# Kernel optimization log

Measured on AMD Instinct MI355X. Metric: run time of the kernel, lower is better.

## Reference

```python
import jax, jax.numpy as jnp
import numpy as np

N = 100000   # nodes
C = 128      # channels
K = 16       # clusters
E = 3200000  # edges (avg degree 32)


def setup_inputs() -> dict:
    key = jax.random.key(0)
    k1, k2, k3, k4 = jax.random.split(key, 4)
    features = jax.random.normal(k1, (N, C), dtype=jnp.float32)
    edge_row = jax.random.randint(k2, (E,), 0, N, dtype=jnp.int32)
    edge_col = jax.random.randint(k3, (E,), 0, N, dtype=jnp.int32)
    edge_val = jnp.ones((E,), dtype=jnp.float32)
    # orthogonal-ish init for fc weight (matches nn.init.orthogonal_ in spirit)
    w = jax.random.normal(k4, (K, C), dtype=jnp.float32)
    q, _ = jnp.linalg.qr(w.T)          # [C, K], orthonormal columns
    fc_w = q.T.astype(jnp.float32)     # [K, C]
    fc_b = jnp.zeros((K,), dtype=jnp.float32)
    return {"features": features, "edge_row": edge_row, "edge_col": edge_col,
            "edge_val": edge_val, "fc_w": fc_w, "fc_b": fc_b}


def reference(features, edge_row, edge_col, edge_val, fc_w, fc_b):
    collapse_regularization = 1.0
    n_nodes = features.shape[0]
    n_clusters = fc_w.shape[0]

    # assignments = softmax(Linear(features))  -> [N, K]
    assignments = jax.nn.softmax(features @ fc_w.T + fc_b, axis=1)
    cluster_sizes = jnp.sum(assignments, axis=0)            # [K]
    assignments_pooling = assignments / cluster_sizes       # [N, K]

    # degrees = column sums of sparse adjacency (no densification)
    degrees = jax.ops.segment_sum(edge_val, edge_col, num_segments=n_nodes)  # [N]
    number_of_edges = jnp.sum(degrees)

    # sparse A @ assignments via segment_sum over edges -> [N, K]
    a_s = jax.ops.segment_sum(edge_val[:, None] * assignments[edge_col],
                              edge_row, num_segments=n_nodes)
    graph_pooled = a_s.T @ assignments                      # S^T A S, [K, K]

    normalizer_left = assignments.T @ degrees[:, None]      # [K, 1]
    normalizer_right = degrees[None, :] @ assignments       # [1, K]
    normalizer = (normalizer_left @ normalizer_right) / 2.0 / number_of_edges

    spectral_loss = -jnp.trace(graph_pooled - normalizer) / 2.0 / number_of_edges
    sk = np.sqrt(n_clusters).astype(np.float32)
    collapse_loss = (jnp.sum(jnp.abs(cluster_sizes - n_nodes / n_clusters))
                     / n_nodes * sk / (sk - 1.0) / 2.0)
    loss = spectral_loss + collapse_regularization * collapse_loss

    features_pooled = jax.nn.selu(assignments_pooling.T @ features)  # [K, C]
    features_pooled = assignments_pooling @ features_pooled          # unpool [N, C]
    return features_pooled, assignments, loss
```

## Files before the change

### kernel.cpp

```cpp
#include <hip/hip_runtime.h>
#include <hip/hip_fp16.h>
#include <math.h>


#define WS_ESUM 0
#define WS_TR   1
#define WS_M    2
#define WS_CS   18
#define WS_B    64

#define OFF_AH  0
#define OFF_CSP 800000
#define OFF_EP  825008
#define OFF_BP  861872

#define GE_BLOCKS 2048
#define GB_BLOCKS 512

typedef int   int4v   __attribute__((ext_vector_type(4)));
typedef float float2v __attribute__((ext_vector_type(2)));
typedef float float4v __attribute__((ext_vector_type(4)));

__global__ __launch_bounds__(256) void k_assign(
    const float* __restrict__ F, const float* __restrict__ W,
    const float* __restrict__ bias, float* __restrict__ A,
    __half* __restrict__ Ah, float* __restrict__ csp, int N) {
  __shared__ float Ws[16 * 144];
  __shared__ float csred[4][16];
  int t = threadIdx.x;
#pragma unroll
  for (int i = 0; i < 8; i++) {
    int idx = t + 256 * i;
    int k = idx >> 7, r = idx & 127;
    Ws[k * 144 + (r >> 5) * 36 + (r & 31)] = W[idx];
  }
  __syncthreads();

  int p = t & 3;
  int slot = t >> 2;
  int n0 = blockIdx.x * 128 + slot;
  int n1 = n0 + 64;
  bool act0 = (n0 < N), act1 = (n1 < N);
  int n0c = act0 ? n0 : (N - 1);
  int n1c = act1 ? n1 : (N - 1);

  float a0[16], a1[16];
#pragma unroll
  for (int k = 0; k < 16; k++) { a0[k] = 0.f; a1[k] = 0.f; }

  const float4* f0 = (const float4*)(F + (size_t)n0c * 128 + p * 32);
  const float4* f1 = (const float4*)(F + (size_t)n1c * 128 + p * 32);
#pragma unroll
  for (int i = 0; i < 8; i++) {
    float4 x0 = f0[i];
    float4 x1 = f1[i];
#pragma unroll
    for (int k = 0; k < 16; k++) {
      float4 w = *(const float4*)(&Ws[k * 144 + p * 36 + i * 4]);
      a0[k] = fmaf(x0.x, w.x, a0[k]);
      a0[k] = fmaf(x0.y, w.y, a0[k]);
      a0[k] = fmaf(x0.z, w.z, a0[k]);
      a0[k] = fmaf(x0.w, w.w, a0[k]);
      a1[k] = fmaf(x1.x, w.x, a1[k]);
      a1[k] = fmaf(x1.y, w.y, a1[k]);
      a1[k] = fmaf(x1.z, w.z, a1[k]);
      a1[k] = fmaf(x1.w, w.w, a1[k]);
    }
  }

#pragma unroll
  for (int k = 0; k < 16; k++) {
    a0[k] += __shfl_xor(a0[k], 1, 64);
    a0[k] += __shfl_xor(a0[k], 2, 64);
    a1[k] += __shfl_xor(a1[k], 1, 64);
    a1[k] += __shfl_xor(a1[k], 2, 64);
  }

#pragma unroll
  for (int k = 0; k < 16; k++) { a0[k] += bias[k]; a1[k] += bias[k]; }

  float mx0 = a0[0], mx1 = a1[0];
#pragma unroll
  for (int k = 1; k < 16; k++) { mx0 = fmaxf(mx0, a0[k]); mx1 = fmaxf(mx1, a1[k]); }
  float s0 = 0.f, s1 = 0.f;
#pragma unroll
  for (int k = 0; k < 16; k++) {
    a0[k] = __expf(a0[k] - mx0); s0 += a0[k];
    a1[k] = __expf(a1[k] - mx1); s1 += a1[k];
  }
  float inv0 = 1.0f / s0, inv1 = 1.0f / s1;
#pragma unroll
  for (int k = 0; k < 16; k++) { a0[k] *= inv0; a1[k] *= inv1; }

  if (act0)
    ((float4*)(A + (size_t)n0 * 16))[p] =
        make_float4(a0[p * 4 + 0], a0[p * 4 + 1], a0[p * 4 + 2], a0[p * 4 + 3]);
  if (act1)
    ((float4*)(A + (size_t)n1 * 16))[p] =
        make_float4(a1[p * 4 + 0], a1[p * 4 + 1], a1[p * 4 + 2], a1[p * 4 + 3]);

  if (p == 0 && act0) {
    __half2 hh[4];
    hh[0].x = __float2half_rn(a0[0]); hh[0].y = __float2half_rn(a0[1]);
    hh[1].x = __float2half_rn(a0[2]); hh[1].y = __float2half_rn(a0[3]);
    hh[2].x = __float2half_rn(a0[4]); hh[2].y = __float2half_rn(a0[5]);
    hh[3].x = __float2half_rn(a0[6]); hh[3].y = __float2half_rn(a0[7]);
    *(uint4*)(Ah + (size_t)n0 * 16) = *(uint4*)hh;
  } else if (p == 1 && act0) {
    __half2 hh[4];
    hh[0].x = __float2half_rn(a0[8]);  hh[0].y = __float2half_rn(a0[9]);
    hh[1].x = __float2half_rn(a0[10]); hh[1].y = __float2half_rn(a0[11]);
    hh[2].x = __float2half_rn(a0[12]); hh[2].y = __float2half_rn(a0[13]);
    hh[3].x = __float2half_rn(a0[14]); hh[3].y = __float2half_rn(a0[15]);
    *(uint4*)(Ah + (size_t)n0 * 16 + 8) = *(uint4*)hh;
  } else if (p == 2 && act1) {
    __half2 hh[4];
    hh[0].x = __float2half_rn(a1[0]); hh[0].y = __float2half_rn(a1[1]);
    hh[1].x = __float2half_rn(a1[2]); hh[1].y = __float2half_rn(a1[3]);
    hh[2].x = __float2half_rn(a1[4]); hh[2].y = __float2half_rn(a1[5]);
    hh[3].x = __float2half_rn(a1[6]); hh[3].y = __float2half_rn(a1[7]);
    *(uint4*)(Ah + (size_t)n1 * 16) = *(uint4*)hh;
  } else if (p == 3 && act1) {
    __half2 hh[4];
    hh[0].x = __float2half_rn(a1[8]);  hh[0].y = __float2half_rn(a1[9]);
    hh[1].x = __float2half_rn(a1[10]); hh[1].y = __float2half_rn(a1[11]);
    hh[2].x = __float2half_rn(a1[12]); hh[2].y = __float2half_rn(a1[13]);
    hh[3].x = __float2half_rn(a1[14]); hh[3].y = __float2half_rn(a1[15]);
    *(uint4*)(Ah + (size_t)n1 * 16 + 8) = *(uint4*)hh;
  }

  int lane = t & 63, wid = t >> 6;
#pragma unroll
  for (int k = 0; k < 16; k++) {
    float v = 0.f;
    if (p == 0) {
      if (act0) v += a0[k];
      if (act1) v += a1[k];
    }
    for (int off = 32; off; off >>= 1) v += __shfl_xor(v, off, 64);
    if (lane == 0) csred[wid][k] = v;
  }
  __syncthreads();
  if (t < 16)
    csp[(size_t)blockIdx.x * 16 + t] =
        csred[0][t] + csred[1][t] + csred[2][t] + csred[3][t];
}

union H2F4 { float4 f4; __half2 h2[4]; };

__device__ __forceinline__ void edge_body(
    const __half* __restrict__ Ah, int r, int c, float v,
    float& eS, float& tr, float* m) {
  const float4* pc = (const float4*)(Ah + (size_t)c * 16);
  const float4* pr = (const float4*)(Ah + (size_t)r * 16);
  H2F4 uc0, uc1, ur0, ur1;
  uc0.f4 = pc[0]; uc1.f4 = pc[1];
  ur0.f4 = pr[0]; ur1.f4 = pr[1];
  float cf[16], rf[16];
#pragma unroll
  for (int j = 0; j < 4; j++) {
    float2 f;
    f = __half22float2(uc0.h2[j]); cf[2 * j] = f.x; cf[2 * j + 1] = f.y;
    f = __half22float2(uc1.h2[j]); cf[8 + 2 * j] = f.x; cf[9 + 2 * j] = f.y;
    f = __half22float2(ur0.h2[j]); rf[2 * j] = f.x; rf[2 * j + 1] = f.y;
    f = __half22float2(ur1.h2[j]); rf[8 + 2 * j] = f.x; rf[9 + 2 * j] = f.y;
  }
  eS += v;
  float d = 0.f;
#pragma unroll
  for (int k = 0; k < 16; k++) {
    m[k] = fmaf(v, cf[k], m[k]);
    d = fmaf(rf[k], cf[k], d);
  }
  tr = fmaf(v, d, tr);
}

__global__ __launch_bounds__(256, 8) void k_edge_nodeB(
    const int* __restrict__ row, const int* __restrict__ col,
    const float* __restrict__ val, const __half* __restrict__ Ah,
    const float* __restrict__ F, const float* __restrict__ A,
    float* __restrict__ ep, float* __restrict__ bp, int E, int N) {
  __shared__ float red[4][18];
  int b = blockIdx.x;
  int t = threadIdx.x;
  bool isNode = ((b % 5) == 4);

  if (!isNode) {
    int eb = b - b / 5;
    float eS = 0.f, tr = 0.f;
    float m[16];
#pragma unroll
    for (int i = 0; i < 16; i++) m[i] = 0.f;

    int tid = eb * 256 + t;
    const int T = GE_BLOCKS * 256;
    int e = tid;
    for (; e + T < E; e += 2 * T) {
      int   r0 = __builtin_nontemporal_load(row + e);
      int   c0 = __builtin_nontemporal_load(col + e);
      int   r1 = __builtin_nontemporal_load(row + e + T);
      int   c1 = __builtin_nontemporal_load(col + e + T);
      float v0 = __builtin_nontemporal_load(val + e);
      float v1 = __builtin_nontemporal_load(val + e + T);
      edge_body(Ah, r0, c0, v0, eS, tr, m);
      edge_body(Ah, r1, c1, v1, eS, tr, m);
    }
    for (; e < E; e += T)
      edge_body(Ah, row[e], col[e], val[e], eS, tr, m);

    float vals[18];
    vals[0] = eS; vals[1] = tr;
#pragma unroll
    for (int i = 0; i < 16; i++) vals[2 + i] = m[i];
#pragma unroll
    for (int i = 0; i < 18; i++) {
      float v = vals[i];
      for (int off = 32; off; off >>= 1) v += __shfl_xor(v, off, 64);
      vals[i] = v;
    }
    int lane = t & 63, wid = t >> 6;
    if (lane == 0) {
#pragma unroll
      for (int i = 0; i < 18; i++) red[wid][i] = vals[i];
    }
    __syncthreads();
    if (t < 18)
      ep[(size_t)eb * 18 + t] =
          red[0][t] + red[1][t] + red[2][t] + red[3][t];
  } else {
    int nb = b / 5;
    int lane = t & 63;
    int wid = t >> 6;

    float2 acc[16];
#pragma unroll
    for (int k = 0; k < 16; k++) acc[k] = make_float2(0.f, 0.f);

    const float2v* F2 = (const float2v*)F;
    const float4* A4 = (const float4*)A;
    const int stride = GB_BLOCKS * 4;
    for (int n = nb * 4 + wid; n < N; n += stride) {
      float2v f = __builtin_nontemporal_load(&F2[(size_t)n * 64 + lane]);
      float4 a0 = A4[(size_t)n * 4 + 0];
      float4 a1 = A4[(size_t)n * 4 + 1];
      float4 a2 = A4[(size_t)n * 4 + 2];
      float4 a3 = A4[(size_t)n * 4 + 3];
      float av[16] = {a0.x, a0.y, a0.z, a0.w, a1.x, a1.y, a1.z, a1.w,
                      a2.x, a2.y, a2.z, a2.w, a3.x, a3.y, a3.z, a3.w};
#pragma unroll
      for (int k = 0; k < 16; k++) {
        acc[k].x = fmaf(av[k], f.x, acc[k].x);
        acc[k].y = fmaf(av[k], f.y, acc[k].y);
      }
    }
    float* myrow = bp + (size_t)(nb * 4 + wid) * 2048;
#pragma unroll
    for (int k = 0; k < 16; k++)
      *(float2*)&myrow[k * 128 + lane * 2] = acc[k];
  }
}

__global__ __launch_bounds__(256) void k_reduce(
    const float* __restrict__ csp, const float* __restrict__ ep,
    const float* __restrict__ bp, float* __restrict__ ws,
    int GA, int GE, int GB) {
  __shared__ float L[256];
  int t = threadIdx.x;
  int b = blockIdx.x;
  if (b < 256) {
    int cell = b * 8 + (t & 7);
    int seg = t >> 3;
    float s0 = 0.f, s1 = 0.f, s2 = 0.f, s3 = 0.f;
    int g = seg;
    for (; g + 96 < GB; g += 128) {
      s0 += bp[(size_t)g * 2048 + cell];
      s1 += bp[(size_t)(g + 32) * 2048 + cell];
      s2 += bp[(size_t)(g + 64) * 2048 + cell];
      s3 += bp[(size_t)(g + 96) * 2048 + cell];
    }
    for (; g < GB; g += 32) s0 += bp[(size_t)g * 2048 + cell];
    L[t] = (s0 + s1) + (s2 + s3);
    __syncthreads();
    if (t < 8) {
      float tot = 0.f;
#pragma unroll
      for (int s = 0; s < 32; s++) tot += L[s * 8 + t];
      ws[WS_B + b * 8 + t] = tot;
    }
  } else if (b == 256) {
    int n = GE * 18;
    float s0 = 0.f, s1 = 0.f, s2 = 0.f, s3 = 0.f;
    if (t < 252) {
      int f = t;
      for (; f + 756 < n; f += 1008) {
        s0 += ep[f]; s1 += ep[f + 252]; s2 += ep[f + 504]; s3 += ep[f + 756];
      }
      for (; f < n; f += 252) s0 += ep[f];
    }
    L[t] = (s0 + s1) + (s2 + s3);
    __syncthreads();
    if (t < 18) {
      float tot = 0.f;
#pragma unroll
      for (int j = 0; j < 14; j++) tot += L[j * 18 + t];
      ws[t] = tot;
    }
  } else {
    int n = GA * 16;
    float s0 = 0.f, s1 = 0.f, s2 = 0.f, s3 = 0.f;
    int f = t;
    for (; f + 768 < n; f += 1024) {
      s0 += csp[f]; s1 += csp[f + 256]; s2 += csp[f + 512]; s3 += csp[f + 768];
    }
    for (; f < n; f += 256) s0 += csp[f];
    L[t] = (s0 + s1) + (s2 + s3);
    __syncthreads();
    if (t < 16) {
      float tot = 0.f;
#pragma unroll
      for (int j = 0; j < 16; j++) tot += L[j * 16 + t];
      ws[WS_CS + t] = tot;
    }
  }
}

__global__ __launch_bounds__(256) void k_unpool(
    const float* __restrict__ A, float* __restrict__ ws,
    float* __restrict__ out, float* __restrict__ loss_out, int N) {
  __shared__ float Ps[2048];
  __shared__ float invcs[16];
  int t = threadIdx.x;
  if (t < 16) invcs[t] = 1.0f / ws[WS_CS + t];
  __syncthreads();
  const float scale = 1.0507009873554805f;
  const float alpha = 1.6732632423543772f;
#pragma unroll
  for (int i = 0; i < 8; i++) {
    int idx = t + 256 * i;
    int k = idx >> 7;
    float x = ws[WS_B + idx] * invcs[k];
    float s = (x > 0.f) ? scale * x : scale * alpha * expm1f(x);
    Ps[idx] = s * invcs[k];
  }
  __syncthreads();

  if (blockIdx.x == 0 && t == 0) {
    float Es = ws[WS_ESUM], tr = ws[WS_TR];
    float m2 = 0.f;
#pragma unroll
    for (int i = 0; i < 16; i++) m2 += ws[WS_M + i] * ws[WS_M + i];
    float spectral = -(tr - m2 / (2.0f * Es)) / (2.0f * Es);
    float coll = 0.f;
    float tgt = (float)N / 16.0f;
#pragma unroll
    for (int i = 0; i < 16; i++) coll += fabsf(ws[WS_CS + i] - tgt);
    coll = coll / (float)N * (4.0f / 3.0f / 2.0f);
    loss_out[0] = spectral + coll;
  }

  int c4 = (t & 31) << 2;
  int sub = t >> 5;
  float4 pk[16];
#pragma unroll
  for (int k = 0; k < 16; k++) pk[k] = *(const float4*)&Ps[k * 128 + c4];

  int stride = gridDim.x * 8;
  for (int n = blockIdx.x * 8 + sub; n < N; n += stride) {
    const float4* a4 = (const float4*)(A + (size_t)n * 16);
    float4 a0 = a4[0], a1 = a4[1], a2 = a4[2], a3 = a4[3];
    float av[16] = {a0.x, a0.y, a0.z, a0.w, a1.x, a1.y, a1.z, a1.w,
                    a2.x, a2.y, a2.z, a2.w, a3.x, a3.y, a3.z, a3.w};
    float4v s = {0.f, 0.f, 0.f, 0.f};
#pragma unroll
    for (int k = 0; k < 16; k++) {
      s.x = fmaf(av[k], pk[k].x, s.x);
      s.y = fmaf(av[k], pk[k].y, s.y);
      s.z = fmaf(av[k], pk[k].z, s.z);
      s.w = fmaf(av[k], pk[k].w, s.w);
    }
    __builtin_nontemporal_store(s, (float4v*)(out + (size_t)n * 128 + c4));
  }
}

extern "C" void kernel_launch(void* const* d_in, const int* in_sizes, int n_in,
                              void* d_out, int out_size, void* d_ws, size_t ws_size,
                              hipStream_t stream) {
  const float* F    = (const float*)d_in[0];
  const int*   erow = (const int*)d_in[1];
  const int*   ecol = (const int*)d_in[2];
  const float* eval_= (const float*)d_in[3];
  const float* W    = (const float*)d_in[4];
  const float* bias = (const float*)d_in[5];

  int N = in_sizes[0] / 128;
  int E = in_sizes[1];

  float* out0 = (float*)d_out;
  float* A    = out0 + (size_t)N * 128;
  float* loss = A + (size_t)N * 16;
  float* ws   = (float*)d_ws;

  int GA = (N + 127) / 128;
  int GE = GE_BLOCKS;
  int GBp = GB_BLOCKS * 4;

  __half* Ah  = (__half*)(out0 + OFF_AH);
  float*  csp = out0 + OFF_CSP;
  float*  ep  = out0 + OFF_EP;
  float*  bp  = out0 + OFF_BP;

  k_assign<<<GA, 256, 0, stream>>>(F, W, bias, A, Ah, csp, N);
  k_edge_nodeB<<<GE_BLOCKS + GB_BLOCKS, 256, 0, stream>>>(
      erow, ecol, eval_, Ah, F, A, ep, bp, E, N);
  k_reduce<<<258, 256, 0, stream>>>(csp, ep, bp, ws, GA, GE, GBp);
  k_unpool<<<1280, 256, 0, stream>>>(A, ws, out0, loss, N);
}
```

Before: 246.8 us.

## Split each edge across two lanes, each handling half of the cluster columns

Each edge is now processed by a pair of adjacent threads, each loading one 16-byte half of the row and column fp16 assignment vectors and accumulating 8 of the 16 cluster sums. This halves per-thread registers and gives more threads and memory requests in flight for the latency-bound gathers. In exchange, the row, col and val index loads are duplicated across the two lanes, and the reduction is restructured to keep the parities separate. eS is halved to correct for the double count.

```diff
diff --git a/kernel.cpp b/kernel.cpp
--- a/kernel.cpp
+++ b/kernel.cpp
@@ -148,27 +148,29 @@
 
 union H2F4 { float4 f4; __half2 h2[4]; };
 
-__device__ __forceinline__ void edge_body(
-    const __half* __restrict__ Ah, int r, int c, float v,
-    float& eS, float& tr, float* m) {
-  const float4* pc = (const float4*)(Ah + (size_t)c * 16);
-  const float4* pr = (const float4*)(Ah + (size_t)r * 16);
-  H2F4 uc0, uc1, ur0, ur1;
-  uc0.f4 = pc[0]; uc1.f4 = pc[1];
-  ur0.f4 = pr[0]; ur1.f4 = pr[1];
-  float cf[16], rf[16];
+__device__ __forceinline__ void pair_body(
+    const __half* __restrict__ Ah, const int* __restrict__ row,
+    const int* __restrict__ col, const float* __restrict__ val,
+    int e, int par, float& eS, float& tr, float* m) {
+  int   r = __builtin_nontemporal_load(row + e);
+  int   c = __builtin_nontemporal_load(col + e);
+  float v = __builtin_nontemporal_load(val + e);
+  const float4* pc = (const float4*)(Ah + ((size_t)c << 4) + (par << 3));
+  const float4* pr = (const float4*)(Ah + ((size_t)r << 4) + (par << 3));
+  H2F4 uc, ur;
+  uc.f4 = *pc;
+  ur.f4 = *pr;
+  float cf[8], rf[8];
 #pragma unroll
   for (int j = 0; j < 4; j++) {
     float2 f;
-    f = __half22float2(uc0.h2[j]); cf[2 * j] = f.x; cf[2 * j + 1] = f.y;
-    f = __half22float2(uc1.h2[j]); cf[8 + 2 * j] = f.x; cf[9 + 2 * j] = f.y;
-    f = __half22float2(ur0.h2[j]); rf[2 * j] = f.x; rf[2 * j + 1] = f.y;
-    f = __half22float2(ur1.h2[j]); rf[8 + 2 * j] = f.x; rf[9 + 2 * j] = f.y;
+    f = __half22float2(uc.h2[j]); cf[2 * j] = f.x; cf[2 * j + 1] = f.y;
+    f = __half22float2(ur.h2[j]); rf[2 * j] = f.x; rf[2 * j + 1] = f.y;
   }
   eS += v;
   float d = 0.f;
 #pragma unroll
-  for (int k = 0; k < 16; k++) {
+  for (int k = 0; k < 8; k++) {
     m[k] = fmaf(v, cf[k], m[k]);
     d = fmaf(rf[k], cf[k], d);
   }
@@ -187,41 +189,45 @@
 
   if (!isNode) {
     int eb = b - b / 5;
+    int par = t & 1;
     float eS = 0.f, tr = 0.f;
-    float m[16];
-#pragma unroll
-    for (int i = 0; i < 16; i++) m[i] = 0.f;
-
-    int tid = eb * 256 + t;
-    const int T = GE_BLOCKS * 256;
-    int e = tid;
-    for (; e + T < E; e += 2 * T) {
-      int   r0 = __builtin_nontemporal_load(row + e);
-      int   c0 = __builtin_nontemporal_load(col + e);
-      int   r1 = __builtin_nontemporal_load(row + e + T);
-      int   c1 = __builtin_nontemporal_load(col + e + T);
-      float v0 = __builtin_nontemporal_load(val + e);
-      float v1 = __builtin_nontemporal_load(val + e + T);
-      edge_body(Ah, r0, c0, v0, eS, tr, m);
-      edge_body(Ah, r1, c1, v1, eS, tr, m);
-    }
-    for (; e < E; e += T)
-      edge_body(Ah, row[e], col[e], val[e], eS, tr, m);
-
-    float vals[18];
-    vals[0] = eS; vals[1] = tr;
-#pragma unroll
-    for (int i = 0; i < 16; i++) vals[2 + i] = m[i];
-#pragma unroll
-    for (int i = 0; i < 18; i++) {
-      float v = vals[i];
-      for (int off = 32; off; off >>= 1) v += __shfl_xor(v, off, 64);
-      vals[i] = v;
+    float m[8];
+#pragma unroll
+    for (int i = 0; i < 8; i++) m[i] = 0.f;
+
+    int pid = eb * 128 + (t >> 1);
+    const int P = GE_BLOCKS * 128;
+    int e = pid;
+    for (; e + P < E; e += 2 * P) {
+      pair_body(Ah, row, col, val, e, par, eS, tr, m);
+      pair_body(Ah, row, col, val, e + P, par, eS, tr, m);
+    }
+    for (; e < E; e += P)
+      pair_body(Ah, row, col, val, e, par, eS, tr, m);
+
+#pragma unroll
+    for (int i = 0; i < 8; i++) {
+      float v = m[i];
+      v += __shfl_xor(v, 32, 64);
+      v += __shfl_xor(v, 16, 64);
+      v += __shfl_xor(v, 8, 64);
+      v += __shfl_xor(v, 4, 64);
+      v += __shfl_xor(v, 2, 64);
+      m[i] = v;
+    }
+    for (int off = 32; off; off >>= 1) {
+      eS += __shfl_xor(eS, off, 64);
+      tr += __shfl_xor(tr, off, 64);
     }
     int lane = t & 63, wid = t >> 6;
     if (lane == 0) {
-#pragma unroll
-      for (int i = 0; i < 18; i++) red[wid][i] = vals[i];
+      red[wid][0] = eS * 0.5f;
+      red[wid][1] = tr;
+#pragma unroll
+      for (int i = 0; i < 8; i++) red[wid][2 + i] = m[i];
+    } else if (lane == 1) {
+#pragma unroll
+      for (int i = 0; i < 8; i++) red[wid][10 + i] = m[i];
     }
     __syncthreads();
     if (t < 18)
```

Measured after the change: 248.2 us. About the same (+0.5%).

## Store assignment copy in FP8 for edge gathers and rebalance assign kernel

Applied to the files above, without the earlier changes.

The compact assignment copy used by the edge kernel is now packed as FP8 (16 bytes per node) instead of FP16 (32 bytes), which halves the random-gather traffic per edge endpoint and uses hardware pack/unpack conversions. k_assign now uses 8 threads per node pair with 64 nodes per block, so there are more blocks and each thread loads less data. The unpool grid is also enlarged. FP8 cuts precision of the trace term in the loss, which may hurt accuracy, and the grid changes alter csp sizing and the reduce partial count.

```diff
diff --git a/kernel.cpp b/kernel.cpp
--- a/kernel.cpp
+++ b/kernel.cpp
@@ -9,7 +9,7 @@
 #define WS_CS   18
 #define WS_B    64
 
-#define OFF_AH  0
+#define OFF_A8  0
 #define OFF_CSP 800000
 #define OFF_EP  825008
 #define OFF_BP  861872
@@ -17,29 +17,29 @@
 #define GE_BLOCKS 2048
 #define GB_BLOCKS 512
 
-typedef int   int4v   __attribute__((ext_vector_type(4)));
 typedef float float2v __attribute__((ext_vector_type(2)));
 typedef float float4v __attribute__((ext_vector_type(4)));
+typedef float f32x2   __attribute__((ext_vector_type(2)));
 
 __global__ __launch_bounds__(256) void k_assign(
     const float* __restrict__ F, const float* __restrict__ W,
     const float* __restrict__ bias, float* __restrict__ A,
-    __half* __restrict__ Ah, float* __restrict__ csp, int N) {
-  __shared__ float Ws[16 * 144];
+    unsigned char* __restrict__ A8, float* __restrict__ csp, int N) {
+  __shared__ float Ws[16 * 160];
   __shared__ float csred[4][16];
   int t = threadIdx.x;
 #pragma unroll
   for (int i = 0; i < 8; i++) {
     int idx = t + 256 * i;
     int k = idx >> 7, r = idx & 127;
-    Ws[k * 144 + (r >> 5) * 36 + (r & 31)] = W[idx];
+    Ws[k * 160 + (r >> 4) * 20 + (r & 15)] = W[idx];
   }
   __syncthreads();
 
-  int p = t & 3;
-  int slot = t >> 2;
-  int n0 = blockIdx.x * 128 + slot;
-  int n1 = n0 + 64;
+  int p = t & 7;
+  int slot = t >> 3;
+  int n0 = blockIdx.x * 64 + slot;
+  int n1 = n0 + 32;
   bool act0 = (n0 < N), act1 = (n1 < N);
   int n0c = act0 ? n0 : (N - 1);
   int n1c = act1 ? n1 : (N - 1);
@@ -48,15 +48,15 @@
 #pragma unroll
   for (int k = 0; k < 16; k++) { a0[k] = 0.f; a1[k] = 0.f; }
 
-  const float4* f0 = (const float4*)(F + (size_t)n0c * 128 + p * 32);
-  const float4* f1 = (const float4*)(F + (size_t)n1c * 128 + p * 32);
-#pragma unroll
-  for (int i = 0; i < 8; i++) {
+  const float4* f0 = (const float4*)(F + (size_t)n0c * 128 + p * 16);
+  const float4* f1 = (const float4*)(F + (size_t)n1c * 128 + p * 16);
+#pragma unroll
+  for (int i = 0; i < 4; i++) {
     float4 x0 = f0[i];
     float4 x1 = f1[i];
 #pragma unroll
     for (int k = 0; k < 16; k++) {
-      float4 w = *(const float4*)(&Ws[k * 144 + p * 36 + i * 4]);
+      float4 w = *(const float4*)(&Ws[k * 160 + p * 20 + i * 4]);
       a0[k] = fmaf(x0.x, w.x, a0[k]);
       a0[k] = fmaf(x0.y, w.y, a0[k]);
       a0[k] = fmaf(x0.z, w.z, a0[k]);
@@ -72,8 +72,10 @@
   for (int k = 0; k < 16; k++) {
     a0[k] += __shfl_xor(a0[k], 1, 64);
     a0[k] += __shfl_xor(a0[k], 2, 64);
+    a0[k] += __shfl_xor(a0[k], 4, 64);
     a1[k] += __shfl_xor(a1[k], 1, 64);
     a1[k] += __shfl_xor(a1[k], 2, 64);
+    a1[k] += __shfl_xor(a1[k], 4, 64);
   }
 
 #pragma unroll
@@ -92,51 +94,47 @@
 #pragma unroll
   for (int k = 0; k < 16; k++) { a0[k] *= inv0; a1[k] *= inv1; }
 
-  if (act0)
-    ((float4*)(A + (size_t)n0 * 16))[p] =
-        make_float4(a0[p * 4 + 0], a0[p * 4 + 1], a0[p * 4 + 2], a0[p * 4 + 3]);
-  if (act1)
-    ((float4*)(A + (size_t)n1 * 16))[p] =
-        make_float4(a1[p * 4 + 0], a1[p * 4 + 1], a1[p * 4 + 2], a1[p * 4 + 3]);
+  if (p < 4) {
+    if (act0)
+      ((float4*)(A + (size_t)n0 * 16))[p] =
+          make_float4(a0[p * 4 + 0], a0[p * 4 + 1], a0[p * 4 + 2], a0[p * 4 + 3]);
+  } else {
+    int q = p - 4;
+    if (act1)
+      ((float4*)(A + (size_t)n1 * 16))[q] =
+          make_float4(a1[q * 4 + 0], a1[q * 4 + 1], a1[q * 4 + 2], a1[q * 4 + 3]);
+  }
 
   if (p == 0 && act0) {
-    __half2 hh[4];
-    hh[0].x = __float2half_rn(a0[0]); hh[0].y = __float2half_rn(a0[1]);
-    hh[1].x = __float2half_rn(a0[2]); hh[1].y = __float2half_rn(a0[3]);
-    hh[2].x = __float2half_rn(a0[4]); hh[2].y = __float2half_rn(a0[5]);
-    hh[3].x = __float2half_rn(a0[6]); hh[3].y = __float2half_rn(a0[7]);
-    *(uint4*)(Ah + (size_t)n0 * 16) = *(uint4*)hh;
-  } else if (p == 1 && act0) {
-    __half2 hh[4];
-    hh[0].x = __float2half_rn(a0[8]);  hh[0].y = __float2half_rn(a0[9]);
-    hh[1].x = __float2half_rn(a0[10]); hh[1].y = __float2half_rn(a0[11]);
-    hh[2].x = __float2half_rn(a0[12]); hh[2].y = __float2half_rn(a0[13]);
-    hh[3].x = __float2half_rn(a0[14]); hh[3].y = __float2half_rn(a0[15]);
-    *(uint4*)(Ah + (size_t)n0 * 16 + 8) = *(uint4*)hh;
-  } else if (p == 2 && act1) {
-    __half2 hh[4];
-    hh[0].x = __float2half_rn(a1[0]); hh[0].y = __float2half_rn(a1[1]);
-    hh[1].x = __float2half_rn(a1[2]); hh[1].y = __float2half_rn(a1[3]);
-    hh[2].x = __float2half_rn(a1[4]); hh[2].y = __float2half_rn(a1[5]);
-    hh[3].x = __float2half_rn(a1[6]); hh[3].y = __float2half_rn(a1[7]);
-    *(uint4*)(Ah + (size_t)n1 * 16) = *(uint4*)hh;
-  } else if (p == 3 && act1) {
-    __half2 hh[4];
-    hh[0].x = __float2half_rn(a1[8]);  hh[0].y = __float2half_rn(a1[9]);
-    hh[1].x = __float2half_rn(a1[10]); hh[1].y = __float2half_rn(a1[11]);
-    hh[2].x = __float2half_rn(a1[12]); hh[2].y = __float2half_rn(a1[13]);
-    hh[3].x = __float2half_rn(a1[14]); hh[3].y = __float2half_rn(a1[15]);
-    *(uint4*)(Ah + (size_t)n1 * 16 + 8) = *(uint4*)hh;
+    uint4 q;
+    q.x = __builtin_amdgcn_cvt_pk_fp8_f32(a0[0],  a0[1],  0u,  false);
+    q.x = __builtin_amdgcn_cvt_pk_fp8_f32(a0[2],  a0[3],  q.x, true);
+    q.y = __builtin_amdgcn_cvt_pk_fp8_f32(a0[4],  a0[5],  0u,  false);
+    q.y = __builtin_amdgcn_cvt_pk_fp8_f32(a0[6],  a0[7],  q.y, true);
+    q.z = __builtin_amdgcn_cvt_pk_fp8_f32(a0[8],  a0[9],  0u,  false);
+    q.z = __builtin_amdgcn_cvt_pk_fp8_f32(a0[10], a0[11], q.z, true);
+    q.w = __builtin_amdgcn_cvt_pk_fp8_f32(a0[12], a0[13], 0u,  false);
+    q.w = __builtin_amdgcn_cvt_pk_fp8_f32(a0[14], a0[15], q.w, true);
+    *(uint4*)(A8 + ((size_t)n0 << 4)) = q;
+  } else if (p == 4 && act1) {
+    uint4 q;
+    q.x = __builtin_amdgcn_cvt_pk_fp8_f32(a1[0],  a1[1],  0u,  false);
+    q.x = __builtin_amdgcn_cvt_pk_fp8_f32(a1[2],  a1[3],  q.x, true);
+    q.y = __builtin_amdgcn_cvt_pk_fp8_f32(a1[4],  a1[5],  0u,  false);
+    q.y = __builtin_amdgcn_cvt_pk_fp8_f32(a1[6],  a1[7],  q.y, true);
+    q.z = __builtin_amdgcn_cvt_pk_fp8_f32(a1[8],  a1[9],  0u,  false);
+    q.z = __builtin_amdgcn_cvt_pk_fp8_f32(a1[10], a1[11], q.z, true);
+    q.w = __builtin_amdgcn_cvt_pk_fp8_f32(a1[12], a1[13], 0u,  false);
+    q.w = __builtin_amdgcn_cvt_pk_fp8_f32(a1[14], a1[15], q.w, true);
+    *(uint4*)(A8 + ((size_t)n1 << 4)) = q;
   }
 
   int lane = t & 63, wid = t >> 6;
 #pragma unroll
   for (int k = 0; k < 16; k++) {
     float v = 0.f;
-    if (p == 0) {
-      if (act0) v += a0[k];
-      if (act1) v += a1[k];
-    }
+    if (p == 0 && act0) v += a0[k];
+    if (p == 4 && act1) v += a1[k];
     for (int off = 32; off; off >>= 1) v += __shfl_xor(v, off, 64);
     if (lane == 0) csred[wid][k] = v;
   }
@@ -146,25 +144,26 @@
         csred[0][t] + csred[1][t] + csred[2][t] + csred[3][t];
 }
 
-union H2F4 { float4 f4; __half2 h2[4]; };
-
-__device__ __forceinline__ void edge_body(
-    const __half* __restrict__ Ah, int r, int c, float v,
+__device__ __forceinline__ void dec16(uint4 q, float* f) {
+  f32x2 a;
+  a = __builtin_amdgcn_cvt_pk_f32_fp8(q.x, false); f[0]  = a[0]; f[1]  = a[1];
+  a = __builtin_amdgcn_cvt_pk_f32_fp8(q.x, true);  f[2]  = a[0]; f[3]  = a[1];
+  a = __builtin_amdgcn_cvt_pk_f32_fp8(q.y, false); f[4]  = a[0]; f[5]  = a[1];
+  a = __builtin_amdgcn_cvt_pk_f32_fp8(q.y, true);  f[6]  = a[0]; f[7]  = a[1];
+  a = __builtin_amdgcn_cvt_pk_f32_fp8(q.z, false); f[8]  = a[0]; f[9]  = a[1];
+  a = __builtin_amdgcn_cvt_pk_f32_fp8(q.z, true);  f[10] = a[0]; f[11] = a[1];
+  a = __builtin_amdgcn_cvt_pk_f32_fp8(q.w, false); f[12] = a[0]; f[13] = a[1];
+  a = __builtin_amdgcn_cvt_pk_f32_fp8(q.w, true);  f[14] = a[0]; f[15] = a[1];
+}
+
+__device__ __forceinline__ void edge_body8(
+    const unsigned char* __restrict__ A8, int r, int c, float v,
     float& eS, float& tr, float* m) {
-  const float4* pc = (const float4*)(Ah + (size_t)c * 16);
-  const float4* pr = (const float4*)(Ah + (size_t)r * 16);
-  H2F4 uc0, uc1, ur0, ur1;
-  uc0.f4 = pc[0]; uc1.f4 = pc[1];
-  ur0.f4 = pr[0]; ur1.f4 = pr[1];
+  uint4 qc = *(const uint4*)(A8 + ((size_t)c << 4));
+  uint4 qr = *(const uint4*)(A8 + ((size_t)r << 4));
   float cf[16], rf[16];
-#pragma unroll
-  for (int j = 0; j < 4; j++) {
-    float2 f;
-    f = __half22float2(uc0.h2[j]); cf[2 * j] = f.x; cf[2 * j + 1] = f.y;
-    f = __half22float2(uc1.h2[j]); cf[8 + 2 * j] = f.x; cf[9 + 2 * j] = f.y;
-    f = __half22float2(ur0.h2[j]); rf[2 * j] = f.x; rf[2 * j + 1] = f.y;
-    f = __half22float2(ur1.h2[j]); rf[8 + 2 * j] = f.x; rf[9 + 2 * j] = f.y;
-  }
+  dec16(qc, cf);
+  dec16(qr, rf);
   eS += v;
   float d = 0.f;
 #pragma unroll
@@ -177,7 +176,7 @@
 
 __global__ __launch_bounds__(256, 8) void k_edge_nodeB(
     const int* __restrict__ row, const int* __restrict__ col,
-    const float* __restrict__ val, const __half* __restrict__ Ah,
+    const float* __restrict__ val, const unsigned char* __restrict__ A8,
     const float* __restrict__ F, const float* __restrict__ A,
     float* __restrict__ ep, float* __restrict__ bp, int E, int N) {
   __shared__ float red[4][18];
@@ -202,11 +201,11 @@
       int   c1 = __builtin_nontemporal_load(col + e + T);
       float v0 = __builtin_nontemporal_load(val + e);
       float v1 = __builtin_nontemporal_load(val + e + T);
-      edge_body(Ah, r0, c0, v0, eS, tr, m);
-      edge_body(Ah, r1, c1, v1, eS, tr, m);
+      edge_body8(A8, r0, c0, v0, eS, tr, m);
+      edge_body8(A8, r1, c1, v1, eS, tr, m);
     }
     for (; e < E; e += T)
-      edge_body(Ah, row[e], col[e], val[e], eS, tr, m);
+      edge_body8(A8, row[e], col[e], val[e], eS, tr, m);
 
     float vals[18];
     vals[0] = eS; vals[1] = tr;
@@ -400,18 +399,18 @@
   float* loss = A + (size_t)N * 16;
   float* ws   = (float*)d_ws;
 
-  int GA = (N + 127) / 128;
+  int GA = (N + 63) / 64;
   int GE = GE_BLOCKS;
   int GBp = GB_BLOCKS * 4;
 
-  __half* Ah  = (__half*)(out0 + OFF_AH);
-  float*  csp = out0 + OFF_CSP;
-  float*  ep  = out0 + OFF_EP;
-  float*  bp  = out0 + OFF_BP;
-
-  k_assign<<<GA, 256, 0, stream>>>(F, W, bias, A, Ah, csp, N);
+  unsigned char* A8 = (unsigned char*)(out0 + OFF_A8);
+  float* csp = out0 + OFF_CSP;
+  float* ep  = out0 + OFF_EP;
+  float* bp  = out0 + OFF_BP;
+
+  k_assign<<<GA, 256, 0, stream>>>(F, W, bias, A, A8, csp, N);
   k_edge_nodeB<<<GE_BLOCKS + GB_BLOCKS, 256, 0, stream>>>(
-      erow, ecol, eval_, Ah, F, A, ep, bp, E, N);
+      erow, ecol, eval_, A8, F, A, ep, bp, E, N);
   k_reduce<<<258, 256, 0, stream>>>(csp, ep, bp, ws, GA, GE, GBp);
-  k_unpool<<<1280, 256, 0, stream>>>(A, ws, out0, loss, N);
-}
+  k_unpool<<<2048, 256, 0, stream>>>(A, ws, out0, loss, N);
+}
```

New measurement: 268.6 us. 1.09x slower.
